# Kernel tuning notes

Measured on AMD Instinct MI355X. Metric: run time of the kernel, lower is better.

The kernel has to match this reference:

```python
import jax, jax.numpy as jnp
import numpy as np

H = 16
DH = 64


def setup_inputs() -> dict:
    key = jax.random.key(0)
    ks = jax.random.split(key, 8)
    b, n, m, d = 2, 2048, 2048, 1024
    inner = H * DH  # 1024
    return {
        "x": jax.random.normal(ks[0], (b, n, d), jnp.float32),
        "mem_k": jax.random.normal(ks[1], (b, m, inner), jnp.float32),
        "mem_v": jax.random.normal(ks[2], (b, m, inner), jnp.float32),
        "Wq": jax.random.normal(ks[3], (d, inner), jnp.float32) * (d ** -0.5),
        "Wkv": jax.random.normal(ks[4], (d, 2 * inner), jnp.float32) * (d ** -0.5),
        "b_kv": jax.random.normal(ks[5], (2 * inner,), jnp.float32) * 0.02,
        "Wo": jax.random.normal(ks[6], (inner, d), jnp.float32) * (inner ** -0.5),
        "b_o": jax.random.normal(ks[7], (d,), jnp.float32) * 0.02,
    }


def reference(x, mem_k, mem_v, Wq, Wkv, b_kv, Wo, b_o):
    b, n, d = x.shape
    scale = DH ** -0.5
    q = (x @ Wq) * scale                       # [b, n, h*dh]
    self_k, self_v = jnp.split(x @ Wkv + b_kv, 2, axis=-1)
    k = jnp.concatenate([mem_k, self_k], axis=1)   # [b, j, h*dh]
    v = jnp.concatenate([mem_v, self_v], axis=1)

    def split_heads(t):
        return t.reshape(b, t.shape[1], H, DH).transpose(0, 2, 1, 3)  # b h n d

    q, k, v = map(split_heads, (q, k, v))
    sim = jnp.einsum('bhid,bhjd->bhij', q, k)  # [b, h, n, j]
    i, j = sim.shape[-2:]
    # causal mask: query i may attend to keys up to position (j - i) + i
    causal_mask = jnp.triu(jnp.ones((i, j), dtype=bool), k=j - i + 1)
    mask_value = -jnp.finfo(sim.dtype).max
    sim = jnp.where(causal_mask[None, None], mask_value, sim)
    attn = jax.nn.softmax(sim, axis=-1)
    out = jnp.einsum('bhij,bhjd->bhid', attn, v)
    out = out.transpose(0, 2, 1, 3).reshape(b, n, H * DH)
    return out @ Wo + b_o
```

## Files before the change

### kernel.cpp

```cpp
#include <hip/hip_runtime.h>
#include <stdint.h>

typedef __bf16 bf16x8 __attribute__((ext_vector_type(8)));
typedef _Float16 f16x8 __attribute__((ext_vector_type(8)));
typedef float f32x4 __attribute__((ext_vector_type(4)));
typedef float f32x16 __attribute__((ext_vector_type(16)));

constexpr int Mm = 2048;
constexpr float QSCALE = 0.18033688011112042f;

__device__ __forceinline__ float exp2_fast(float x) {
  return __builtin_amdgcn_exp2f(x);
}

__device__ __forceinline__ uint16_t f2bf(float f) {
  union { float f; uint32_t u; } v; v.f = f;
  return (uint16_t)((v.u + 0x7FFFu + ((v.u >> 16) & 1u)) >> 16);
}
__device__ __forceinline__ uint32_t pack2(float a, float b) {
  return (uint32_t)f2bf(a) | ((uint32_t)f2bf(b) << 16);
}
__device__ __forceinline__ uint32_t pkrtz(float a, float b) {
  auto h2 = __builtin_amdgcn_cvt_pkrtz(a, b);
  return __builtin_bit_cast(uint32_t, h2);
}
__device__ __forceinline__ uint16_t f2h(float f) {
  _Float16 h = (_Float16)f;
  return __builtin_bit_cast(uint16_t, h);
}

__device__ __forceinline__ void async16(const void* g, void* l) {
  __builtin_amdgcn_global_load_lds(
      (__attribute__((address_space(1))) uint32_t*)g,
      (__attribute__((address_space(3))) uint32_t*)l, 16, 0, 0);
}

__device__ __forceinline__ bf16x8 frag64(const uint16_t* base, int row, int chunk) {
  return *(const bf16x8*)(base + row * 64 + chunk * 8);
}
__device__ __forceinline__ f16x8 frag64h(const uint16_t* base, int row, int chunk) {
  return *(const f16x8*)(base + row * 64 + chunk * 8);
}

__global__ __launch_bounds__(256) void prep_kernel(
    const float* __restrict__ x, const float* __restrict__ mem_k,
    const float* __restrict__ mem_v, const float* __restrict__ Wq,
    const float* __restrict__ Wkv, const float* __restrict__ Wo,
    uint16_t* __restrict__ Xb, uint16_t* __restrict__ WallT,
    uint16_t* __restrict__ WoT, uint16_t* __restrict__ Kh,
    uint16_t* __restrict__ VhT) {
  __shared__ float tile[64][65];
  __shared__ uint16_t vtile[64 * 66];
  const int tid = threadIdx.x;
  int blk = blockIdx.x;

  if (blk < 1024) {
    const float4* x4 = (const float4*)x;
    for (int it = 0; it < 4; ++it) {
      int idx4 = blk * 1024 + it * 256 + tid;
      float4 v = x4[idx4];
      uint2 w; w.x = pack2(v.x, v.y); w.y = pack2(v.z, v.w);
      ((uint2*)Xb)[idx4] = w;
    }
    return;
  }
  blk -= 1024;
  if (blk < 1024) {
    const float* src; uint16_t* dst; int ld, colbase, n0, k0;
    if (blk < 768) {
      int nt = blk >> 4, kt = blk & 15;
      n0 = nt * 64; k0 = kt * 64;
      if (n0 < 1024) { src = Wq; ld = 1024; colbase = n0; }
      else           { src = Wkv; ld = 2048; colbase = n0 - 1024; }
      dst = WallT;
    } else {
      int b2 = blk - 768;
      int nt = b2 >> 4, kt = b2 & 15;
      n0 = nt * 64; k0 = kt * 64;
      src = Wo; ld = 1024; colbase = n0; dst = WoT;
    }
    int r = tid >> 4, c = (tid & 15) * 4;
    for (int it = 0; it < 4; ++it) {
      int rr = r + it * 16;
      float4 v = *(const float4*)(src + (size_t)(k0 + rr) * ld + colbase + c);
      tile[rr][c] = v.x; tile[rr][c + 1] = v.y;
      tile[rr][c + 2] = v.z; tile[rr][c + 3] = v.w;
    }
    __syncthreads();
    for (int it = 0; it < 4; ++it) {
      int rn = r + it * 16;
      uint2 w;
      w.x = pack2(tile[c][rn], tile[c + 1][rn]);
      w.y = pack2(tile[c + 2][rn], tile[c + 3][rn]);
      *(uint2*)(dst + (size_t)(n0 + rn) * 1024 + k0 + c) = w;
    }
    return;
  }
  blk -= 1024;
  if (blk < 1024) {
    const float4* s4 = (const float4*)mem_k;
    for (int it = 0; it < 4; ++it) {
      int idx4 = blk * 1024 + it * 256 + tid;
      int e = idx4 * 4;
      int b = e >> 21;
      int rem = e & ((1 << 21) - 1);
      int m = rem >> 10;
      int cc = rem & 1023;
      int h = cc >> 6, dh = cc & 63;
      float4 v = s4[idx4];
      uint2 w; w.x = pack2(v.x, v.y); w.y = pack2(v.z, v.w);
      *(uint2*)(Kh + (((size_t)(b * 16 + h) * 4096) + m) * 64 + dh) = w;
    }
    return;
  }
  blk -= 1024;
  {
    const int b = blk >> 9, h = (blk >> 5) & 15, m0 = (blk & 31) * 64;
    const float4* s4 = (const float4*)mem_v;
    for (int it = 0; it < 4; ++it) {
      int idx = it * 256 + tid;
      int r = idx >> 4, d4 = (idx & 15) * 4;
      float4 v = s4[(size_t)(b * 2048 + m0 + r) * 256 + h * 16 + (d4 >> 2)];
      *(uint32_t*)&vtile[r * 66 + d4]     = pkrtz(v.x, v.y);
      *(uint32_t*)&vtile[r * 66 + d4 + 2] = pkrtz(v.z, v.w);
    }
    __syncthreads();
    for (int it2 = 0; it2 < 2; ++it2) {
      int chunk = it2 * 256 + tid;
      int d = chunk >> 3, mg = chunk & 7;
      uint32_t w[4];
      for (int p = 0; p < 4; ++p) {
        uint32_t lo = vtile[(mg * 8 + 2 * p) * 66 + d];
        uint32_t hi = vtile[(mg * 8 + 2 * p + 1) * 66 + d];
        w[p] = lo | (hi << 16);
      }
      *(uint4*)&VhT[((size_t)((b * 16 + h) * 64) + d) * 4096 + m0 + mg * 8] =
          *(uint4*)w;
    }
  }
}

template <int MODE>
__global__ __launch_bounds__(256) void gemm_kernel(
    const uint16_t* __restrict__ A, const uint16_t* __restrict__ Bt,
    const float* __restrict__ bias, uint16_t* __restrict__ Qh,
    uint16_t* __restrict__ Kh, uint16_t* __restrict__ VhT,
    float* __restrict__ Out) {
  constexpr int K = 1024;
  constexpr int SS = 136;
  constexpr int BM = (MODE == 0) ? 128 : 64;
  constexpr int MT = BM / 32;
  constexpr int CPT = (BM + 128) * 8 / 256;
  const int m0 = blockIdx.x * BM, n0 = blockIdx.y * 128;
  const int tid = threadIdx.x;
  const int wave = tid >> 6, lane = tid & 63;
  const int lhi = lane >> 4, llo = lane & 15;
  const int wm = (wave >> 1) * (BM / 2), wn = (wave & 1) * 64;

  __shared__ uint16_t sh[MODE == 0 ? 128 * SS : 16896];
  uint16_t* As = sh;
  uint16_t* Bs = sh + BM * 64;

  f32x4 acc[MT][4] = {};

  for (int kt = 0; kt < K / 64; ++kt) {
    __syncthreads();
    for (int c = 0; c < CPT; ++c) {
      int cl = c * 256 + tid;
      if (cl < BM * 8) {
        int row = cl >> 3, ch = cl & 7;
        async16(A + (size_t)(m0 + row) * K + kt * 64 + ch * 8, As + cl * 8);
      } else {
        int bl = cl - BM * 8;
        int row = bl >> 3, ch = bl & 7;
        async16(Bt + (size_t)(n0 + row) * K + kt * 64 + ch * 8, Bs + bl * 8);
      }
    }
    __syncthreads();
    for (int ks = 0; ks < 2; ++ks) {
      bf16x8 af[MT], bfr[4];
      for (int mt = 0; mt < MT; ++mt) af[mt] = frag64(As, wm + mt * 16 + llo, ks * 4 + lhi);
      for (int nt = 0; nt < 4; ++nt) bfr[nt] = frag64(Bs, wn + nt * 16 + llo, ks * 4 + lhi);
      for (int mt = 0; mt < MT; ++mt)
        for (int nt = 0; nt < 4; ++nt)
          acc[mt][nt] = __builtin_amdgcn_mfma_f32_16x16x32_bf16(af[mt], bfr[nt], acc[mt][nt], 0, 0, 0);
    }
  }

  if (MODE == 0) {
    const int region = n0 >> 10;
    __syncthreads();
    for (int nt = 0; nt < 4; ++nt) {
      int cloc = wn + nt * 16 + llo;
      int col = n0 + cloc;
      float badd = (region == 0) ? 0.f : bias[col - 1024];
      for (int mt = 0; mt < 4; ++mt) {
        int rloc = wm + mt * 16 + lhi * 4;
        for (int reg = 0; reg < 4; ++reg) {
          float v = acc[mt][nt][reg];
          v = (region == 0) ? v * QSCALE : v + badd;
          if (region == 2) sh[cloc * SS + rloc + reg] = f2h(v);
          else             sh[(rloc + reg) * SS + cloc] = f2bf(v);
        }
      }
    }
    __syncthreads();
    if (region == 2) {
      const int rl = (tid & 15) * 8;
      for (int it = 0; it < 8; ++it) {
        int cloc = (tid >> 4) + it * 16;
        int col = n0 + cloc;
        int cc = col - 2048, h = cc >> 6, dh = cc & 63;
        int r = m0 + rl;
        int b = r >> 11, n = r & 2047;
        uint4 w = *(const uint4*)&sh[cloc * SS + rl];
        *(uint4*)&VhT[((size_t)((b * 16 + h) * 64) + dh) * 4096 + 2048 + n] = w;
      }
    } else {
      const int cl16 = (tid & 15) * 8;
      const int col = n0 + cl16;
      for (int it = 0; it < 8; ++it) {
        int rloc = (tid >> 4) + it * 16;
        int r = m0 + rloc;
        int b = r >> 11, n = r & 2047;
        uint4 w = *(const uint4*)&sh[rloc * SS + cl16];
        if (region == 0) {
          int h = col >> 6, dh = col & 63;
          *(uint4*)&Qh[(((size_t)(b * 16 + h) * 2048) + n) * 64 + dh] = w;
        } else {
          int cc = col - 1024, h = cc >> 6, dh = cc & 63;
          *(uint4*)&Kh[(((size_t)(b * 16 + h) * 4096) + 2048 + n) * 64 + dh] = w;
        }
      }
    }
  } else {
    __syncthreads();
    float* shf = (float*)sh;
    for (int nt = 0; nt < 4; ++nt) {
      int cloc = wn + nt * 16 + llo;
      float bo = bias[n0 + cloc];
      for (int mt = 0; mt < MT; ++mt) {
        int rloc = wm + mt * 16 + lhi * 4;
        for (int reg = 0; reg < 4; ++reg)
          shf[(rloc + reg) * 132 + cloc] = acc[mt][nt][reg] + bo;
      }
    }
    __syncthreads();
    for (int it = 0; it < 8; ++it) {
      int chunk = it * 256 + tid;
      int row = chunk >> 5, c4 = chunk & 31;
      float4 v = *(const float4*)&shf[row * 132 + c4 * 4];
      *(float4*)&Out[(size_t)(m0 + row) * 1024 + n0 + c4 * 4] = v;
    }
  }
}

__global__ __launch_bounds__(256, 2) void attn_kernel(
    const uint16_t* __restrict__ Qh, const uint16_t* __restrict__ Kh,
    const uint16_t* __restrict__ VhT, uint16_t* __restrict__ AO) {
  const int bh = blockIdx.x;
  const int qt = (blockIdx.y < 8) ? (15 - (int)blockIdx.y)
                                  : ((int)blockIdx.y - 8);
  const int tid = threadIdx.x;
  const int wave = tid >> 6, lane = tid & 63;
  const int lo5 = lane & 31, hi = lane >> 5;
  const int qg = wave & 1, kp = wave >> 1;
  const int i0 = qt * 128;
  const int swz5 = lo5 & 7;

  __shared__ uint16_t Ks[2][2][64 * 64];
  __shared__ uint16_t Vt[2][2][64 * 64];

  bf16x8 qf0[4], qf1[4];
  {
    const uint16_t* Qw0 = Qh + ((size_t)bh * 2048 + i0 + qg * 64 + lo5) * 64;
    const uint16_t* Qw1 = Qw0 + 32 * 64;
#pragma unroll
    for (int k = 0; k < 4; ++k) {
      qf0[k] = *(const bf16x8*)(Qw0 + k * 16 + hi * 8);
      qf1[k] = *(const bf16x8*)(Qw1 + k * 16 + hi * 8);
    }
  }

  const uint16_t* Kbh = Kh + (size_t)bh * 4096 * 64;
  const uint16_t* Vbh = VhT + (size_t)bh * 64 * 4096;

  f32x16 o00 = {}, o01 = {}, o10 = {}, o11 = {};
  float l0p = 0.f, l1p = 0.f;

  const int npairs = 17 + qt;

  auto stage = [&](int buf, int u_) {
    const int arr = wave >> 1;
    const int par = wave & 1;
    const int kk0 = u_ * 128 + par * 64;
    uint16_t* dstb = arr == 0 ? &Ks[buf][par][0] : &Vt[buf][par][0];
#pragma unroll
    for (int c = 0; c < 8; ++c) {
      int row = c * 8 + (lane >> 3);
      int chs = (lane & 7) ^ (row & 7);
      const uint16_t* src = arr == 0
          ? Kbh + (size_t)(kk0 + row) * 64 + chs * 8
          : Vbh + (size_t)row * 4096 + kk0 + chs * 8;
      async16(src, dstb + c * 512);
    }
  };

  stage(0, 0);

  const int iw0 = i0 + qg * 64;
  const int iw1 = iw0 + 32;

  for (int u = 0; u < npairs; ++u) {
    const int cur = u & 1;
    __syncthreads();
    if (u + 1 < npairs) stage(cur ^ 1, u + 1);

    const int k0t = (2 * u + kp) * 64;
    const uint16_t* Kt = &Ks[cur][kp][0];
    const uint16_t* Vtt = &Vt[cur][kp][0];

    uint32_t pw0[2][2][4], pw1[2][2][4];

#pragma unroll
    for (int mblk = 0; mblk < 2; ++mblk) {
      f32x16 s0v = {}, s1v = {};
      __builtin_amdgcn_s_setprio(1);
#pragma unroll
      for (int kstep = 0; kstep < 4; ++kstep) {
        bf16x8 kf = frag64(Kt, mblk * 32 + lo5, (2 * kstep + hi) ^ swz5);
        s0v = __builtin_amdgcn_mfma_f32_32x32x16_bf16(kf, qf0[kstep], s0v, 0, 0, 0);
        s1v = __builtin_amdgcn_mfma_f32_32x32x16_bf16(kf, qf1[kstep], s1v, 0, 0, 0);
      }
      __builtin_amdgcn_s_setprio(0);

      if (k0t + mblk * 32 + 31 > Mm + iw0) {
        const int lim = Mm + iw0 + lo5 - k0t - mblk * 32;
#pragma unroll
        for (int r = 0; r < 16; ++r) {
          int kl = (r & 3) + 8 * (r >> 2) + 4 * hi;
          if (kl > lim) s0v[r] = -INFINITY;
        }
      }
      if (k0t + mblk * 32 + 31 > Mm + iw1) {
        const int lim = Mm + iw1 + lo5 - k0t - mblk * 32;
#pragma unroll
        for (int r = 0; r < 16; ++r) {
          int kl = (r & 3) + 8 * (r >> 2) + 4 * hi;
          if (kl > lim) s1v[r] = -INFINITY;
        }
      }

      uint32_t c0[8], c1[8];
#pragma unroll
      for (int w = 0; w < 8; ++w) {
        float a0 = exp2_fast(s0v[2 * w]), a1 = exp2_fast(s0v[2 * w + 1]);
        c0[w] = pkrtz(a0, a1);
        l0p += a0 + a1;
        float b0 = exp2_fast(s1v[2 * w]), b1 = exp2_fast(s1v[2 * w + 1]);
        c1[w] = pkrtz(b0, b1);
        l1p += b0 + b1;
      }
#pragma unroll
      for (int kk2 = 0; kk2 < 2; ++kk2) {
        uint32_t a0 = c0[4 * kk2 + 0], a2 = c0[4 * kk2 + 2];
        uint32_t a1 = c0[4 * kk2 + 1], a3 = c0[4 * kk2 + 3];
        asm volatile("v_permlane32_swap_b32 %0, %1" : "+v"(a0), "+v"(a2));
        asm volatile("v_permlane32_swap_b32 %0, %1" : "+v"(a1), "+v"(a3));
        pw0[mblk][kk2][0] = a0; pw0[mblk][kk2][1] = a1;
        pw0[mblk][kk2][2] = a2; pw0[mblk][kk2][3] = a3;
        uint32_t b0 = c1[4 * kk2 + 0], b2 = c1[4 * kk2 + 2];
        uint32_t b1 = c1[4 * kk2 + 1], b3 = c1[4 * kk2 + 3];
        asm volatile("v_permlane32_swap_b32 %0, %1" : "+v"(b0), "+v"(b2));
        asm volatile("v_permlane32_swap_b32 %0, %1" : "+v"(b1), "+v"(b3));
        pw1[mblk][kk2][0] = b0; pw1[mblk][kk2][1] = b1;
        pw1[mblk][kk2][2] = b2; pw1[mblk][kk2][3] = b3;
      }
    }

#pragma unroll
    for (int mblk = 0; mblk < 2; ++mblk)
#pragma unroll
      for (int kk2 = 0; kk2 < 2; ++kk2) {
        const int kk = mblk * 2 + kk2;
        uint4 fwa; fwa.x = pw0[mblk][kk2][0]; fwa.y = pw0[mblk][kk2][1];
        fwa.z = pw0[mblk][kk2][2]; fwa.w = pw0[mblk][kk2][3];
        f16x8 pa0 = __builtin_bit_cast(f16x8, fwa);
        uint4 fwb; fwb.x = pw1[mblk][kk2][0]; fwb.y = pw1[mblk][kk2][1];
        fwb.z = pw1[mblk][kk2][2]; fwb.w = pw1[mblk][kk2][3];
        f16x8 pa1 = __builtin_bit_cast(f16x8, fwb);
        f16x8 vf0 = frag64h(Vtt, lo5,      (2 * kk + hi) ^ swz5);
        f16x8 vf1 = frag64h(Vtt, 32 + lo5, (2 * kk + hi) ^ swz5);
        __builtin_amdgcn_s_setprio(1);
        o00 = __builtin_amdgcn_mfma_f32_32x32x16_f16(pa0, vf0, o00, 0, 0, 0);
        o01 = __builtin_amdgcn_mfma_f32_32x32x16_f16(pa0, vf1, o01, 0, 0, 0);
        o10 = __builtin_amdgcn_mfma_f32_32x32x16_f16(pa1, vf0, o10, 0, 0, 0);
        o11 = __builtin_amdgcn_mfma_f32_32x32x16_f16(pa1, vf1, o11, 0, 0, 0);
        __builtin_amdgcn_s_setprio(0);
      }
  }

  float l0full, l1full;
  {
    float a0 = l0p, b0 = l0p;
    asm volatile("v_permlane32_swap_b32 %0, %1" : "+v"(a0), "+v"(b0));
    l0full = a0 + b0;
    float a1 = l1p, b1 = l1p;
    asm volatile("v_permlane32_swap_b32 %0, %1" : "+v"(a1), "+v"(b1));
    l1full = a1 + b1;
  }

  const int b = bh >> 4, h = bh & 15;
  float* F = (float*)&Ks[0][0][0];
  float* L = (float*)&Vt[1][0][0];
  uint16_t* Es = &Vt[0][0][0];

  __syncthreads();
  if (hi == 0) {
    L[kp * 128 + qg * 64 + lo5]      = l0full;
    L[kp * 128 + qg * 64 + 32 + lo5] = l1full;
  }
  if (kp == 1) {
#pragma unroll
    for (int r = 0; r < 16; ++r) {
      int q0 = qg * 64 + (r & 3) + 8 * (r >> 2) + 4 * hi;
      int q1 = q0 + 32;
      F[q0 * 64 + lo5]      = o00[r];
      F[q0 * 64 + 32 + lo5] = o01[r];
      F[q1 * 64 + lo5]      = o10[r];
      F[q1 * 64 + 32 + lo5] = o11[r];
    }
  }
  __syncthreads();
  if (kp == 0) {
#pragma unroll
    for (int r = 0; r < 16; ++r) {
      int q0 = qg * 64 + (r & 3) + 8 * (r >> 2) + 4 * hi;
      int q1 = q0 + 32;
      float inv0 = 1.0f / (L[q0] + L[128 + q0]);
      float inv1 = 1.0f / (L[q1] + L[128 + q1]);
      Es[q0 * 64 + lo5]      = f2bf((o00[r] + F[q0 * 64 + lo5]) * inv0);
      Es[q0 * 64 + 32 + lo5] = f2bf((o01[r] + F[q0 * 64 + 32 + lo5]) * inv0);
      Es[q1 * 64 + lo5]      = f2bf((o10[r] + F[q1 * 64 + lo5]) * inv1);
      Es[q1 * 64 + 32 + lo5] = f2bf((o11[r] + F[q1 * 64 + 32 + lo5]) * inv1);
    }
  }
  __syncthreads();
  {
    int row = tid >> 1, c32 = (tid & 1) * 32;
    size_t base = ((size_t)(b * 2048) + i0 + row) * 1024 + h * 64 + c32;
    *(uint4*)&AO[base]      = *(const uint4*)&Es[row * 64 + c32];
    *(uint4*)&AO[base + 8]  = *(const uint4*)&Es[row * 64 + c32 + 8];
    *(uint4*)&AO[base + 16] = *(const uint4*)&Es[row * 64 + c32 + 16];
    *(uint4*)&AO[base + 24] = *(const uint4*)&Es[row * 64 + c32 + 24];
  }
}

extern "C" void kernel_launch(void* const* d_in, const int* in_sizes, int n_in,
                              void* d_out, int out_size, void* d_ws,
                              size_t ws_size, hipStream_t stream) {
  const float* x     = (const float*)d_in[0];
  const float* mem_k = (const float*)d_in[1];
  const float* mem_v = (const float*)d_in[2];
  const float* Wq    = (const float*)d_in[3];
  const float* Wkv   = (const float*)d_in[4];
  const float* b_kv  = (const float*)d_in[5];
  const float* Wo    = (const float*)d_in[6];
  const float* b_o   = (const float*)d_in[7];
  float* out = (float*)d_out;

  char* ws = (char*)d_ws;
  uint16_t* Xb    = (uint16_t*)(ws);
  uint16_t* WallT = (uint16_t*)(ws + (8ull << 20));
  uint16_t* WoT   = (uint16_t*)(ws + (14ull << 20));
  uint16_t* Qh    = (uint16_t*)(ws + (16ull << 20));
  uint16_t* Kh    = (uint16_t*)(ws + (24ull << 20));
  uint16_t* VhT   = (uint16_t*)(ws + (40ull << 20));
  uint16_t* AO    = (uint16_t*)(ws + (56ull << 20));

  prep_kernel<<<4096, 256, 0, stream>>>(x, mem_k, mem_v, Wq, Wkv, Wo,
                                        Xb, WallT, WoT, Kh, VhT);
  gemm_kernel<0><<<dim3(32, 24), 256, 0, stream>>>(Xb, WallT, b_kv,
                                                   Qh, Kh, VhT, nullptr);
  attn_kernel<<<dim3(32, 16), 256, 0, stream>>>(Qh, Kh, VhT, AO);
  gemm_kernel<1><<<dim3(64, 8), 256, 0, stream>>>(AO, WoT, b_o,
                                                  nullptr, nullptr, nullptr, out);
}
```

Before: 236.3 us.

## Overlap mem_k/mem_v conversion with QKV GEMM in a fused launch

The bf16/f16 conversion and head-layout reshuffle of mem_k and mem_v move out of the prep kernel and into the QKV projection GEMM launch. Blocks are interleaved 3 GEMM tiles to 8 conversion blocks (out of each 11), so the memory-bound conversion runs alongside the compute-bound GEMM tiles. This is meant to hide the conversion traffic behind the GEMM and shrink the prep kernel. In exchange the GEMM blocks share CUs with conversion blocks, and the grid mapping through modulo-11 indexing becomes more complex.

```diff
diff --git a/kernel.cpp b/kernel.cpp
--- a/kernel.cpp
+++ b/kernel.cpp
@@ -43,14 +43,11 @@
 }
 
 __global__ __launch_bounds__(256) void prep_kernel(
-    const float* __restrict__ x, const float* __restrict__ mem_k,
-    const float* __restrict__ mem_v, const float* __restrict__ Wq,
+    const float* __restrict__ x, const float* __restrict__ Wq,
     const float* __restrict__ Wkv, const float* __restrict__ Wo,
     uint16_t* __restrict__ Xb, uint16_t* __restrict__ WallT,
-    uint16_t* __restrict__ WoT, uint16_t* __restrict__ Kh,
-    uint16_t* __restrict__ VhT) {
+    uint16_t* __restrict__ WoT) {
   __shared__ float tile[64][65];
-  __shared__ uint16_t vtile[64 * 66];
   const int tid = threadIdx.x;
   int blk = blockIdx.x;
 
@@ -65,7 +62,7 @@
     return;
   }
   blk -= 1024;
-  if (blk < 1024) {
+  {
     const float* src; uint16_t* dst; int ld, colbase, n0, k0;
     if (blk < 768) {
       int nt = blk >> 4, kt = blk & 15;
@@ -94,61 +91,153 @@
       w.y = pack2(tile[c + 2][rn], tile[c + 3][rn]);
       *(uint2*)(dst + (size_t)(n0 + rn) * 1024 + k0 + c) = w;
     }
-    return;
-  }
-  blk -= 1024;
-  if (blk < 1024) {
-    const float4* s4 = (const float4*)mem_k;
-    for (int it = 0; it < 4; ++it) {
-      int idx4 = blk * 1024 + it * 256 + tid;
-      int e = idx4 * 4;
-      int b = e >> 21;
-      int rem = e & ((1 << 21) - 1);
-      int m = rem >> 10;
-      int cc = rem & 1023;
-      int h = cc >> 6, dh = cc & 63;
-      float4 v = s4[idx4];
-      uint2 w; w.x = pack2(v.x, v.y); w.y = pack2(v.z, v.w);
-      *(uint2*)(Kh + (((size_t)(b * 16 + h) * 4096) + m) * 64 + dh) = w;
-    }
-    return;
-  }
-  blk -= 1024;
-  {
-    const int b = blk >> 9, h = (blk >> 5) & 15, m0 = (blk & 31) * 64;
-    const float4* s4 = (const float4*)mem_v;
-    for (int it = 0; it < 4; ++it) {
-      int idx = it * 256 + tid;
-      int r = idx >> 4, d4 = (idx & 15) * 4;
-      float4 v = s4[(size_t)(b * 2048 + m0 + r) * 256 + h * 16 + (d4 >> 2)];
-      *(uint32_t*)&vtile[r * 66 + d4]     = pkrtz(v.x, v.y);
-      *(uint32_t*)&vtile[r * 66 + d4 + 2] = pkrtz(v.z, v.w);
-    }
-    __syncthreads();
-    for (int it2 = 0; it2 < 2; ++it2) {
-      int chunk = it2 * 256 + tid;
-      int d = chunk >> 3, mg = chunk & 7;
-      uint32_t w[4];
-      for (int p = 0; p < 4; ++p) {
-        uint32_t lo = vtile[(mg * 8 + 2 * p) * 66 + d];
-        uint32_t hi = vtile[(mg * 8 + 2 * p + 1) * 66 + d];
-        w[p] = lo | (hi << 16);
-      }
-      *(uint4*)&VhT[((size_t)((b * 16 + h) * 64) + d) * 4096 + m0 + mg * 8] =
-          *(uint4*)w;
-    }
-  }
-}
-
-template <int MODE>
-__global__ __launch_bounds__(256) void gemm_kernel(
+  }
+}
+
+__global__ __launch_bounds__(256) void gemm0_fused(
     const uint16_t* __restrict__ A, const uint16_t* __restrict__ Bt,
-    const float* __restrict__ bias, uint16_t* __restrict__ Qh,
-    uint16_t* __restrict__ Kh, uint16_t* __restrict__ VhT,
-    float* __restrict__ Out) {
+    const float* __restrict__ bias, const float* __restrict__ mem_k,
+    const float* __restrict__ mem_v, uint16_t* __restrict__ Qh,
+    uint16_t* __restrict__ Kh, uint16_t* __restrict__ VhT) {
   constexpr int K = 1024;
   constexpr int SS = 136;
-  constexpr int BM = (MODE == 0) ? 128 : 64;
+  __shared__ uint16_t sh[128 * SS];
+  const int tid = threadIdx.x;
+  const int bid = blockIdx.x;
+  const int r11 = bid % 11;
+
+  if (r11 >= 3) {
+    const int m = (bid / 11) * 8 + (r11 - 3);
+    if (m < 1024) {
+      const float4* s4 = (const float4*)mem_k;
+      for (int it = 0; it < 4; ++it) {
+        int idx4 = m * 1024 + it * 256 + tid;
+        int e = idx4 * 4;
+        int b = e >> 21;
+        int rem = e & ((1 << 21) - 1);
+        int mm = rem >> 10;
+        int cc = rem & 1023;
+        int h = cc >> 6, dh = cc & 63;
+        float4 v = s4[idx4];
+        uint2 w; w.x = pack2(v.x, v.y); w.y = pack2(v.z, v.w);
+        *(uint2*)(Kh + (((size_t)(b * 16 + h) * 4096) + mm) * 64 + dh) = w;
+      }
+    } else {
+      const int blk = m - 1024;
+      const int b = blk >> 9, h = (blk >> 5) & 15, m0v = (blk & 31) * 64;
+      uint16_t* vtile = sh;
+      const float4* s4 = (const float4*)mem_v;
+      for (int it = 0; it < 4; ++it) {
+        int idx = it * 256 + tid;
+        int r = idx >> 4, d4 = (idx & 15) * 4;
+        float4 v = s4[(size_t)(b * 2048 + m0v + r) * 256 + h * 16 + (d4 >> 2)];
+        *(uint32_t*)&vtile[r * 66 + d4]     = pkrtz(v.x, v.y);
+        *(uint32_t*)&vtile[r * 66 + d4 + 2] = pkrtz(v.z, v.w);
+      }
+      __syncthreads();
+      for (int it2 = 0; it2 < 2; ++it2) {
+        int chunk = it2 * 256 + tid;
+        int d = chunk >> 3, mg = chunk & 7;
+        uint32_t w[4];
+        for (int p = 0; p < 4; ++p) {
+          uint32_t lo = vtile[(mg * 8 + 2 * p) * 66 + d];
+          uint32_t hi = vtile[(mg * 8 + 2 * p + 1) * 66 + d];
+          w[p] = lo | (hi << 16);
+        }
+        *(uint4*)&VhT[((size_t)((b * 16 + h) * 64) + d) * 4096 + m0v + mg * 8] =
+            *(uint4*)w;
+      }
+    }
+    return;
+  }
+
+  const int g = (bid / 11) * 3 + r11;
+  const int m0 = (g & 31) * 128, n0 = (g >> 5) * 128;
+  const int wave = tid >> 6, lane = tid & 63;
+  const int lhi = lane >> 4, llo = lane & 15;
+  const int wm = (wave >> 1) * 64, wn = (wave & 1) * 64;
+
+  uint16_t* As = sh;
+  uint16_t* Bs = sh + 128 * 64;
+
+  f32x4 acc[4][4] = {};
+
+  for (int kt = 0; kt < K / 64; ++kt) {
+    __syncthreads();
+    for (int c = 0; c < 8; ++c) {
+      int cl = c * 256 + tid;
+      if (cl < 128 * 8) {
+        int row = cl >> 3, ch = cl & 7;
+        async16(A + (size_t)(m0 + row) * K + kt * 64 + ch * 8, As + cl * 8);
+      } else {
+        int bl = cl - 128 * 8;
+        int row = bl >> 3, ch = bl & 7;
+        async16(Bt + (size_t)(n0 + row) * K + kt * 64 + ch * 8, Bs + bl * 8);
+      }
+    }
+    __syncthreads();
+    for (int ks = 0; ks < 2; ++ks) {
+      bf16x8 af[4], bfr[4];
+      for (int mt = 0; mt < 4; ++mt) af[mt] = frag64(As, wm + mt * 16 + llo, ks * 4 + lhi);
+      for (int nt = 0; nt < 4; ++nt) bfr[nt] = frag64(Bs, wn + nt * 16 + llo, ks * 4 + lhi);
+      for (int mt = 0; mt < 4; ++mt)
+        for (int nt = 0; nt < 4; ++nt)
+          acc[mt][nt] = __builtin_amdgcn_mfma_f32_16x16x32_bf16(af[mt], bfr[nt], acc[mt][nt], 0, 0, 0);
+    }
+  }
+
+  const int region = n0 >> 10;
+  __syncthreads();
+  for (int nt = 0; nt < 4; ++nt) {
+    int cloc = wn + nt * 16 + llo;
+    int col = n0 + cloc;
+    float badd = (region == 0) ? 0.f : bias[col - 1024];
+    for (int mt = 0; mt < 4; ++mt) {
+      int rloc = wm + mt * 16 + lhi * 4;
+      for (int reg = 0; reg < 4; ++reg) {
+        float v = acc[mt][nt][reg];
+        v = (region == 0) ? v * QSCALE : v + badd;
+        if (region == 2) sh[cloc * SS + rloc + reg] = f2h(v);
+        else             sh[(rloc + reg) * SS + cloc] = f2bf(v);
+      }
+    }
+  }
+  __syncthreads();
+  if (region == 2) {
+    const int rl = (tid & 15) * 8;
+    for (int it = 0; it < 8; ++it) {
+      int cloc = (tid >> 4) + it * 16;
+      int col = n0 + cloc;
+      int cc = col - 2048, h = cc >> 6, dh = cc & 63;
+      int r = m0 + rl;
+      int b = r >> 11, n = r & 2047;
+      uint4 w = *(const uint4*)&sh[cloc * SS + rl];
+      *(uint4*)&VhT[((size_t)((b * 16 + h) * 64) + dh) * 4096 + 2048 + n] = w;
+    }
+  } else {
+    const int cl16 = (tid & 15) * 8;
+    const int col = n0 + cl16;
+    for (int it = 0; it < 8; ++it) {
+      int rloc = (tid >> 4) + it * 16;
+      int r = m0 + rloc;
+      int b = r >> 11, n = r & 2047;
+      uint4 w = *(const uint4*)&sh[rloc * SS + cl16];
+      if (region == 0) {
+        int h = col >> 6, dh = col & 63;
+        *(uint4*)&Qh[(((size_t)(b * 16 + h) * 2048) + n) * 64 + dh] = w;
+      } else {
+        int cc = col - 1024, h = cc >> 6, dh = cc & 63;
+        *(uint4*)&Kh[(((size_t)(b * 16 + h) * 4096) + 2048 + n) * 64 + dh] = w;
+      }
+    }
+  }
+}
+
+__global__ __launch_bounds__(256) void gemm1_kernel(
+    const uint16_t* __restrict__ A, const uint16_t* __restrict__ Bt,
+    const float* __restrict__ bias, float* __restrict__ Out) {
+  constexpr int K = 1024;
+  constexpr int BM = 64;
   constexpr int MT = BM / 32;
   constexpr int CPT = (BM + 128) * 8 / 256;
   const int m0 = blockIdx.x * BM, n0 = blockIdx.y * 128;
@@ -157,7 +246,7 @@
   const int lhi = lane >> 4, llo = lane & 15;
   const int wm = (wave >> 1) * (BM / 2), wn = (wave & 1) * 64;
 
-  __shared__ uint16_t sh[MODE == 0 ? 128 * SS : 16896];
+  __shared__ uint16_t sh[16896];
   uint16_t* As = sh;
   uint16_t* Bs = sh + BM * 64;
 
@@ -187,71 +276,23 @@
     }
   }
 
-  if (MODE == 0) {
-    const int region = n0 >> 10;
-    __syncthreads();
-    for (int nt = 0; nt < 4; ++nt) {
-      int cloc = wn + nt * 16 + llo;
-      int col = n0 + cloc;
-      float badd = (region == 0) ? 0.f : bias[col - 1024];
-      for (int mt = 0; mt < 4; ++mt) {
-        int rloc = wm + mt * 16 + lhi * 4;
-        for (int reg = 0; reg < 4; ++reg) {
-          float v = acc[mt][nt][reg];
-          v = (region == 0) ? v * QSCALE : v + badd;
-          if (region == 2) sh[cloc * SS + rloc + reg] = f2h(v);
-          else             sh[(rloc + reg) * SS + cloc] = f2bf(v);
-        }
-      }
-    }
-    __syncthreads();
-    if (region == 2) {
-      const int rl = (tid & 15) * 8;
-      for (int it = 0; it < 8; ++it) {
-        int cloc = (tid >> 4) + it * 16;
-        int col = n0 + cloc;
-        int cc = col - 2048, h = cc >> 6, dh = cc & 63;
-        int r = m0 + rl;
-        int b = r >> 11, n = r & 2047;
-        uint4 w = *(const uint4*)&sh[cloc * SS + rl];
-        *(uint4*)&VhT[((size_t)((b * 16 + h) * 64) + dh) * 4096 + 2048 + n] = w;
-      }
-    } else {
-      const int cl16 = (tid & 15) * 8;
-      const int col = n0 + cl16;
-      for (int it = 0; it < 8; ++it) {
-        int rloc = (tid >> 4) + it * 16;
-        int r = m0 + rloc;
-        int b = r >> 11, n = r & 2047;
-        uint4 w = *(const uint4*)&sh[rloc * SS + cl16];
-        if (region == 0) {
-          int h = col >> 6, dh = col & 63;
-          *(uint4*)&Qh[(((size_t)(b * 16 + h) * 2048) + n) * 64 + dh] = w;
-        } else {
-          int cc = col - 1024, h = cc >> 6, dh = cc & 63;
-          *(uint4*)&Kh[(((size_t)(b * 16 + h) * 4096) + 2048 + n) * 64 + dh] = w;
-        }
-      }
-    }
-  } else {
-    __syncthreads();
-    float* shf = (float*)sh;
-    for (int nt = 0; nt < 4; ++nt) {
-      int cloc = wn + nt * 16 + llo;
-      float bo = bias[n0 + cloc];
-      for (int mt = 0; mt < MT; ++mt) {
-        int rloc = wm + mt * 16 + lhi * 4;
-        for (int reg = 0; reg < 4; ++reg)
-          shf[(rloc + reg) * 132 + cloc] = acc[mt][nt][reg] + bo;
-      }
-    }
-    __syncthreads();
-    for (int it = 0; it < 8; ++it) {
-      int chunk = it * 256 + tid;
-      int row = chunk >> 5, c4 = chunk & 31;
-      float4 v = *(const float4*)&shf[row * 132 + c4 * 4];
-      *(float4*)&Out[(size_t)(m0 + row) * 1024 + n0 + c4 * 4] = v;
-    }
+  __syncthreads();
+  float* shf = (float*)sh;
+  for (int nt = 0; nt < 4; ++nt) {
+    int cloc = wn + nt * 16 + llo;
+    float bo = bias[n0 + cloc];
+    for (int mt = 0; mt < MT; ++mt) {
+      int rloc = wm + mt * 16 + lhi * 4;
+      for (int reg = 0; reg < 4; ++reg)
+        shf[(rloc + reg) * 132 + cloc] = acc[mt][nt][reg] + bo;
+    }
+  }
+  __syncthreads();
+  for (int it = 0; it < 8; ++it) {
+    int chunk = it * 256 + tid;
+    int row = chunk >> 5, c4 = chunk & 31;
+    float4 v = *(const float4*)&shf[row * 132 + c4 * 4];
+    *(float4*)&Out[(size_t)(m0 + row) * 1024 + n0 + c4 * 4] = v;
   }
 }
 
@@ -478,11 +519,9 @@
   uint16_t* VhT   = (uint16_t*)(ws + (40ull << 20));
   uint16_t* AO    = (uint16_t*)(ws + (56ull << 20));
 
-  prep_kernel<<<4096, 256, 0, stream>>>(x, mem_k, mem_v, Wq, Wkv, Wo,
-                                        Xb, WallT, WoT, Kh, VhT);
-  gemm_kernel<0><<<dim3(32, 24), 256, 0, stream>>>(Xb, WallT, b_kv,
-                                                   Qh, Kh, VhT, nullptr);
+  prep_kernel<<<2048, 256, 0, stream>>>(x, Wq, Wkv, Wo, Xb, WallT, WoT);
+  gemm0_fused<<<2816, 256, 0, stream>>>(Xb, WallT, b_kv, mem_k, mem_v,
+                                        Qh, Kh, VhT);
   attn_kernel<<<dim3(32, 16), 256, 0, stream>>>(Qh, Kh, VhT, AO);
-  gemm_kernel<1><<<dim3(64, 8), 256, 0, stream>>>(AO, WoT, b_o,
-                                                  nullptr, nullptr, nullptr, out);
-}
+  gemm1_kernel<<<dim3(64, 8), 256, 0, stream>>>(AO, WoT, b_o, out);
+}
```

Result: slower. 252.4 us (+6.8%).
